# Kernel optimization log

Hardware: AMD Instinct MI355X
Metric: run time of the kernel (lower is better)

## Reference

```python
import jax, jax.numpy as jnp
import numpy as np

N = 50000        # nodes
E = 800000       # edges (avg degree 16)
H = 128          # hidden_nf
IN_NODE = 11     # in_node_nf
IN_EDGE = 4      # in_edge_nf
L = 4            # n_layers


def _lin_init(key, fan_in, fan_out, layers=None):
    shape = (fan_in, fan_out) if layers is None else (layers, fan_in, fan_out)
    return jax.random.normal(key, shape, dtype=jnp.float32) / np.sqrt(fan_in)


def setup_inputs() -> dict:
    key = jax.random.key(0)
    ks = jax.random.split(key, 16)
    edge_in = 2 * H + 1 + IN_EDGE   # [h_row, h_col, radial, edge_attr]
    node_in = H + H + IN_NODE       # [h, agg, h0]
    return {
        "h0": jax.random.normal(ks[0], (N, IN_NODE), dtype=jnp.float32),
        "x": jax.random.normal(ks[1], (N, 3), dtype=jnp.float32),
        "edge_index": jax.random.randint(ks[2], (2, E), 0, N),
        "edge_attr": jax.random.normal(ks[3], (E, IN_EDGE), dtype=jnp.float32),
        "node_mask": jnp.ones((N, 1), dtype=jnp.float32),
        "edge_mask": jnp.ones((E, 1), dtype=jnp.float32),
        "n_nodes": N,
        "emb_w": _lin_init(ks[4], IN_NODE, H),
        "emb_b": jnp.zeros((H,), dtype=jnp.float32),
        "ew1": _lin_init(ks[5], edge_in, H, L),
        "eb1": jnp.zeros((L, H), dtype=jnp.float32),
        "ew2": _lin_init(ks[6], H, H, L),
        "eb2": jnp.zeros((L, H), dtype=jnp.float32),
        "nw1": _lin_init(ks[7], node_in, H, L),
        "nb1": jnp.zeros((L, H), dtype=jnp.float32),
        "nw2": _lin_init(ks[8], H, H, L),
        "nb2": jnp.zeros((L, H), dtype=jnp.float32),
    }


def reference(h0, x, edge_index, edge_attr, node_mask, edge_mask, n_nodes,
              emb_w, emb_b, ew1, eb1, ew2, eb2, nw1, nb1, nw2, nb2):
    row, col = edge_index[0], edge_index[1]
    num_nodes = h0.shape[0]
    # coord2radial (coords never updated since coord_model is not called)
    coord_diff = x[row] - x[col]                               # [E, 3]
    radial = jnp.sum(coord_diff * coord_diff, axis=1, keepdims=True)  # [E, 1]

    h = h0 @ emb_w + emb_b                                     # embedding, [N, H]
    for i in range(L):
        # edge model
        edge_in = jnp.concatenate([h[row], h[col], radial, edge_attr], axis=1)
        m = jax.nn.silu(edge_in @ ew1[i] + eb1[i])
        m = jax.nn.silu(m @ ew2[i] + eb2[i])
        m = m * edge_mask                                      # [E, H]
        # node model: scatter-sum messages, concat with h and node_attr=h0
        agg = jax.ops.segment_sum(m, row, num_segments=num_nodes)  # [N, H]
        node_in = jnp.concatenate([h, agg, h0], axis=1)
        out = jax.nn.silu(node_in @ nw1[i] + nb1[i]) @ nw2[i] + nb2[i]
        h = h + out                                            # recurrent residual
    return h
```

## Files before the change

### kernel.cpp

```cpp
#include <hip/hip_runtime.h>

#define NN 50000
#define NE 800000
#define HD 128
#define INN 11
#define NL 4
#define NG16 3125
#define BTS 132
#define K1S 292

typedef __attribute__((ext_vector_type(8))) short bf16x8;
typedef __attribute__((ext_vector_type(4))) float f32x4;

__device__ __forceinline__ float silu_f(float x) {
    return x * __builtin_amdgcn_rcpf(1.0f + __expf(-x));
}

__device__ __forceinline__ short f2bf(float x) {
    unsigned u = __float_as_uint(x);
    return (short)((u + 0x7FFFu + ((u >> 16) & 1u)) >> 16);
}
__device__ __forceinline__ unsigned f2bf2u(float lo, float hi) {
    unsigned a = __float_as_uint(lo), b = __float_as_uint(hi);
    a = (a + 0x7FFFu + ((a >> 16) & 1u)) >> 16;
    b = (b + 0x7FFFu + ((b >> 16) & 1u)) & 0xFFFF0000u;
    return a | b;
}
__device__ __forceinline__ bf16x8 pack8(float4 a, float4 b) {
    bf16x8 r;
    r[0] = f2bf(a.x); r[1] = f2bf(a.y); r[2] = f2bf(a.z); r[3] = f2bf(a.w);
    r[4] = f2bf(b.x); r[5] = f2bf(b.y); r[6] = f2bf(b.z); r[7] = f2bf(b.w);
    return r;
}

__global__ __launch_bounds__(256) void embed_kernel(
    const float* __restrict__ h0, const float* __restrict__ w,
    const float* __restrict__ b, float* __restrict__ h)
{
    int idx = blockIdx.x * 256 + threadIdx.x;
    if (idx >= NN * HD) return;
    int n = idx >> 7, j = idx & 127;
    float acc = b[j];
    #pragma unroll
    for (int k = 0; k < INN; ++k)
        acc += h0[n * INN + k] * w[k * HD + j];
    h[idx] = acc;
}

__global__ __launch_bounds__(256) void csr_zero(int* __restrict__ cnt)
{
    int i = blockIdx.x * 256 + threadIdx.x;
    if (i < NN) cnt[i] = 0;
}

__global__ __launch_bounds__(256) void csr_hist(const int* __restrict__ ei, int* __restrict__ cnt)
{
    int e = blockIdx.x * 256 + threadIdx.x;
    atomicAdd(&cnt[ei[e]], 1);
}

__global__ __launch_bounds__(1024) void csr_scan(
    const int* __restrict__ cnt, int* __restrict__ rowptr, int* __restrict__ cursor)
{
    __shared__ int part[1024];
    int t = threadIdx.x;
    int base = t * 49;
    int s = 0;
    for (int i = 0; i < 49; ++i) { int j = base + i; if (j < NN) s += cnt[j]; }
    part[t] = s;
    __syncthreads();
    for (int off = 1; off < 1024; off <<= 1) {
        int v = (t >= off) ? part[t - off] : 0;
        __syncthreads();
        part[t] += v;
        __syncthreads();
    }
    int run = (t == 0) ? 0 : part[t - 1];
    for (int i = 0; i < 49; ++i) {
        int j = base + i;
        if (j < NN) { rowptr[j] = run; cursor[j] = run; run += cnt[j]; }
    }
    if (t == 1023) rowptr[NN] = part[1023];
}

__global__ __launch_bounds__(256) void csr_fill(
    const int* __restrict__ ei, int* __restrict__ cursor, int* __restrict__ eidx)
{
    int e = blockIdx.x * 256 + threadIdx.x;
    int r = ei[e];
    int p = atomicAdd(&cursor[r], 1);
    eidx[p] = e;
}

__global__ __launch_bounds__(256) void edge_pre(
    const int* __restrict__ ei, const int* __restrict__ eidx,
    const float* __restrict__ x, const float* __restrict__ eattr,
    const float* __restrict__ emask,
    int4* __restrict__ ed_p, float4* __restrict__ ea_p)
{
    int p = blockIdx.x * 256 + threadIdx.x;
    int e = eidx[p];
    int r = ei[e], c = ei[NE + e];
    float dx = x[3 * r]     - x[3 * c];
    float dy = x[3 * r + 1] - x[3 * c + 1];
    float dz = x[3 * r + 2] - x[3 * c + 2];
    float rad = dx * dx + dy * dy + dz * dz;
    ed_p[p] = make_int4(r * 64, c * 64, __float_as_int(rad), __float_as_int(emask[e]));
    ea_p[p] = ((const float4*)eattr)[e];
}

__global__ __launch_bounds__(512) void tu_mfma(
    const float* __restrict__ h, const float* __restrict__ ew1_l,
    short* __restrict__ tb, short* __restrict__ ub)
{
    __shared__ __align__(16) short BT[128 * BTS];
    const float* wsrc = ew1_l + (blockIdx.y ? 128 * HD : 0);
    short* outp = blockIdx.y ? ub : tb;
    for (int i = threadIdx.x; i < 128 * 128; i += 512) {
        int c = i >> 7, k = i & 127;
        BT[c * BTS + k] = f2bf(wsrc[k * HD + c]);
    }
    int wv = threadIdx.x >> 6, lane = threadIdx.x & 63;
    int ln15 = lane & 15, quad = lane >> 4;
    __syncthreads();

    for (int g = blockIdx.x * 8 + wv; g < NG16; g += gridDim.x * 8) {
        int row = g * 16 + ln15;
        const float* hrow = h + row * HD;
        bf16x8 afr[4];
        #pragma unroll
        for (int kt = 0; kt < 4; ++kt) {
            float4 x0 = *(const float4*)(hrow + kt * 32 + quad * 8);
            float4 x1 = *(const float4*)(hrow + kt * 32 + quad * 8 + 4);
            afr[kt] = pack8(x0, x1);
        }
        #pragma unroll
        for (int ct = 0; ct < 8; ++ct) {
            f32x4 acc = {0.f, 0.f, 0.f, 0.f};
            #pragma unroll
            for (int kt = 0; kt < 4; ++kt) {
                bf16x8 bfr = *(const bf16x8*)&BT[(ct * 16 + ln15) * BTS + kt * 32 + quad * 8];
                acc = __builtin_amdgcn_mfma_f32_16x16x32_bf16(afr[kt], bfr, acc, 0, 0, 0);
            }
            int col = ct * 16 + ln15;
            #pragma unroll
            for (int r4 = 0; r4 < 4; ++r4) {
                int orow = g * 16 + quad * 4 + r4;
                outp[orow * HD + col] = f2bf(acc[r4]);
            }
        }
    }
}

__global__ __launch_bounds__(512) void edge_m_kernel(
    const short* __restrict__ tb, const short* __restrict__ ub,
    const int4* __restrict__ ed_p, const float4* __restrict__ ea_p,
    const int* __restrict__ rowptr,
    const float* __restrict__ ew1_l, const float* __restrict__ eb1_l,
    const float* __restrict__ ew2_l, const float* __restrict__ eb2_l,
    float* __restrict__ agg)
{
    __shared__ __align__(16) short BT[128 * BTS];
    __shared__ __align__(16) short VA[8][16 * BTS];
    __shared__ float s_b2[128];

    for (int i = threadIdx.x; i < 128 * 128; i += 512) {
        int k = i >> 7, n = i & 127;
        BT[n * BTS + k] = f2bf(ew2_l[i]);
    }
    if (threadIdx.x < 128) s_b2[threadIdx.x] = eb2_l[threadIdx.x];

    int cp = threadIdx.x & 63;
    int c0 = cp * 2;
    float wr0  = ew1_l[256 * HD + c0],     wr1  = ew1_l[256 * HD + c0 + 1];
    float wa00 = ew1_l[257 * HD + c0],     wa01 = ew1_l[257 * HD + c0 + 1];
    float wa10 = ew1_l[258 * HD + c0],     wa11 = ew1_l[258 * HD + c0 + 1];
    float wa20 = ew1_l[259 * HD + c0],     wa21 = ew1_l[259 * HD + c0 + 1];
    float wa30 = ew1_l[260 * HD + c0],     wa31 = ew1_l[260 * HD + c0 + 1];
    float b10  = eb1_l[c0],                b11  = eb1_l[c0 + 1];

    int lane = threadIdx.x & 63;
    int wv   = threadIdx.x >> 6;
    int ln15 = lane & 15;
    int quad = lane >> 4;
    short* VAw = &VA[wv][0];
    const unsigned* tb32 = (const unsigned*)tb;
    const unsigned* ub32 = (const unsigned*)ub;
    __syncthreads();

    for (int n = blockIdx.x * 8 + wv; n < NN; n += gridDim.x * 8) {
        int s = rowptr[n], e = rowptr[n + 1];
        unsigned tw = tb32[n * 64 + cp];
        float t0 = __uint_as_float(tw << 16);
        float t1 = __uint_as_float(tw & 0xFFFF0000u);

        float sums[8];
        #pragma unroll
        for (int ct = 0; ct < 8; ++ct) sums[ct] = 0.f;

        for (int base = s; base < e; base += 16) {
            #pragma unroll 4
            for (int i = 0; i < 16; ++i) {
                int p = base + i;
                unsigned out = 0u;
                if (p < e) {
                    int4   ed = ed_p[p];
                    float4 ea = ea_p[p];
                    float rad = __int_as_float(ed.z);
                    unsigned uw = ub32[ed.y + cp];
                    float u0 = __uint_as_float(uw << 16);
                    float u1 = __uint_as_float(uw & 0xFFFF0000u);
                    float base0 = rad * wr0 + ea.x * wa00 + ea.y * wa10 + ea.z * wa20 + ea.w * wa30 + b10;
                    float base1 = rad * wr1 + ea.x * wa01 + ea.y * wa11 + ea.z * wa21 + ea.w * wa31 + b11;
                    out = f2bf2u(silu_f(t0 + u0 + base0), silu_f(t1 + u1 + base1));
                }
                *(unsigned*)&VAw[i * BTS + c0] = out;
            }

            int pr = base + quad * 4;
            float mk0 = (pr + 0 < e) ? __int_as_float(ed_p[pr + 0].w) : 0.f;
            float mk1 = (pr + 1 < e) ? __int_as_float(ed_p[pr + 1].w) : 0.f;
            float mk2 = (pr + 2 < e) ? __int_as_float(ed_p[pr + 2].w) : 0.f;
            float mk3 = (pr + 3 < e) ? __int_as_float(ed_p[pr + 3].w) : 0.f;

            __builtin_amdgcn_wave_barrier();
            __builtin_amdgcn_s_waitcnt(0xc07f);

            bf16x8 afr[4];
            #pragma unroll
            for (int kt = 0; kt < 4; ++kt)
                afr[kt] = *(const bf16x8*)&VAw[ln15 * BTS + kt * 32 + quad * 8];

            __builtin_amdgcn_wave_barrier();

            #pragma unroll
            for (int ct = 0; ct < 8; ++ct) {
                f32x4 acc = {0.f, 0.f, 0.f, 0.f};
                #pragma unroll
                for (int kt = 0; kt < 4; ++kt) {
                    bf16x8 bfr = *(const bf16x8*)&BT[(ct * 16 + ln15) * BTS + kt * 32 + quad * 8];
                    acc = __builtin_amdgcn_mfma_f32_16x16x32_bf16(afr[kt], bfr, acc, 0, 0, 0);
                }
                float b2c = s_b2[ct * 16 + ln15];
                sums[ct] += silu_f(acc[0] + b2c) * mk0 + silu_f(acc[1] + b2c) * mk1
                          + silu_f(acc[2] + b2c) * mk2 + silu_f(acc[3] + b2c) * mk3;
            }
        }

        #pragma unroll
        for (int ct = 0; ct < 8; ++ct) {
            float v = sums[ct];
            v += __shfl_xor(v, 16, 64);
            v += __shfl_xor(v, 32, 64);
            sums[ct] = v;
        }
        float vA = (quad & 2) ? ((quad & 1) ? sums[6] : sums[4])
                              : ((quad & 1) ? sums[2] : sums[0]);
        float vB = (quad & 2) ? ((quad & 1) ? sums[7] : sums[5])
                              : ((quad & 1) ? sums[3] : sums[1]);
        int colA = quad * 32 + ln15;
        agg[n * HD + colA]      = vA;
        agg[n * HD + colA + 16] = vB;
    }
}

__global__ __launch_bounds__(512) void nk1_mfma(
    const float* __restrict__ h, const float* __restrict__ agg,
    const float* __restrict__ h0,
    const float* __restrict__ nw1_l, const float* __restrict__ nb1_l,
    short* __restrict__ qb)
{
    __shared__ __align__(16) short BT[64 * K1S];
    int c0 = blockIdx.y * 64;
    for (int i = threadIdx.x; i < 64 * 288; i += 512) {
        int c = i / 288, k = i - c * 288;
        BT[c * K1S + k] = (k < 267) ? f2bf(nw1_l[k * HD + c0 + c]) : (short)0;
    }
    int wv = threadIdx.x >> 6, lane = threadIdx.x & 63;
    int ln15 = lane & 15, quad = lane >> 4;
    __syncthreads();

    for (int g = blockIdx.x * 8 + wv; g < NG16; g += gridDim.x * 8) {
        int row = g * 16 + ln15;
        const float* hrow = h + row * HD;
        const float* arow = agg + row * HD;
        bf16x8 afr[9];
        #pragma unroll
        for (int kt = 0; kt < 4; ++kt) {
            float4 x0 = *(const float4*)(hrow + kt * 32 + quad * 8);
            float4 x1 = *(const float4*)(hrow + kt * 32 + quad * 8 + 4);
            afr[kt] = pack8(x0, x1);
        }
        #pragma unroll
        for (int kt = 0; kt < 4; ++kt) {
            float4 x0 = *(const float4*)(arow + kt * 32 + quad * 8);
            float4 x1 = *(const float4*)(arow + kt * 32 + quad * 8 + 4);
            afr[4 + kt] = pack8(x0, x1);
        }
        {
            bf16x8 a8 = {0, 0, 0, 0, 0, 0, 0, 0};
            if (quad == 0) {
                #pragma unroll
                for (int jj = 0; jj < 8; ++jj) a8[jj] = f2bf(h0[row * INN + jj]);
            } else if (quad == 1) {
                #pragma unroll
                for (int jj = 0; jj < 3; ++jj) a8[jj] = f2bf(h0[row * INN + 8 + jj]);
            }
            afr[8] = a8;
        }
        #pragma unroll
        for (int ct = 0; ct < 4; ++ct) {
            f32x4 acc = {0.f, 0.f, 0.f, 0.f};
            #pragma unroll
            for (int kt = 0; kt < 9; ++kt) {
                bf16x8 bfr = *(const bf16x8*)&BT[(ct * 16 + ln15) * K1S + kt * 32 + quad * 8];
                acc = __builtin_amdgcn_mfma_f32_16x16x32_bf16(afr[kt], bfr, acc, 0, 0, 0);
            }
            int col = c0 + ct * 16 + ln15;
            float b = nb1_l[col];
            #pragma unroll
            for (int r4 = 0; r4 < 4; ++r4) {
                int orow = g * 16 + quad * 4 + r4;
                qb[orow * HD + col] = f2bf(silu_f(acc[r4] + b));
            }
        }
    }
}

__global__ __launch_bounds__(512) void nk2_mfma(
    const short* __restrict__ qb, const float* __restrict__ nw2_l,
    const float* __restrict__ nb2_l, float* __restrict__ h)
{
    __shared__ __align__(16) short BT[128 * BTS];
    for (int i = threadIdx.x; i < 128 * 128; i += 512) {
        int c = i >> 7, k = i & 127;
        BT[c * BTS + k] = f2bf(nw2_l[k * HD + c]);
    }
    int wv = threadIdx.x >> 6, lane = threadIdx.x & 63;
    int ln15 = lane & 15, quad = lane >> 4;
    __syncthreads();

    for (int g = blockIdx.x * 8 + wv; g < NG16; g += gridDim.x * 8) {
        int row = g * 16 + ln15;
        bf16x8 afr[4];
        #pragma unroll
        for (int kt = 0; kt < 4; ++kt)
            afr[kt] = *(const bf16x8*)(qb + row * HD + kt * 32 + quad * 8);

        #pragma unroll
        for (int ct = 0; ct < 8; ++ct) {
            f32x4 acc = {0.f, 0.f, 0.f, 0.f};
            #pragma unroll
            for (int kt = 0; kt < 4; ++kt) {
                bf16x8 bfr = *(const bf16x8*)&BT[(ct * 16 + ln15) * BTS + kt * 32 + quad * 8];
                acc = __builtin_amdgcn_mfma_f32_16x16x32_bf16(afr[kt], bfr, acc, 0, 0, 0);
            }
            int col = ct * 16 + ln15;
            float b = nb2_l[col];
            #pragma unroll
            for (int r4 = 0; r4 < 4; ++r4) {
                int orow = g * 16 + quad * 4 + r4;
                h[orow * HD + col] += acc[r4] + b;
            }
        }
    }
}

extern "C" void kernel_launch(void* const* d_in, const int* in_sizes, int n_in,
                              void* d_out, int out_size, void* d_ws, size_t ws_size,
                              hipStream_t stream)
{
    const float* h0    = (const float*)d_in[0];
    const float* x     = (const float*)d_in[1];
    const int*   ei    = (const int*)d_in[2];
    const float* eattr = (const float*)d_in[3];
    const float* emask = (const float*)d_in[5];
    const float* emb_w = (const float*)d_in[7];
    const float* emb_b = (const float*)d_in[8];
    const float* ew1   = (const float*)d_in[9];
    const float* eb1   = (const float*)d_in[10];
    const float* ew2   = (const float*)d_in[11];
    const float* eb2   = (const float*)d_in[12];
    const float* nw1   = (const float*)d_in[13];
    const float* nb1   = (const float*)d_in[14];
    const float* nw2   = (const float*)d_in[15];
    const float* nb2   = (const float*)d_in[16];

    float* h = (float*)d_out;

    short*  tb     = (short*)d_ws;
    short*  ub     = tb + (size_t)NN * HD;
    float*  agg    = (float*)(ub + (size_t)NN * HD);
    short*  qb     = tb;
    int*    cnt    = (int*)(agg + (size_t)NN * HD);
    int*    rowptr = cnt + NN;
    int*    cursor = rowptr + NN + 1;
    int*    eidx   = cursor + NN;
    int4*   ed_p   = (int4*)(eidx + NE + 1);
    float4* ea_p   = (float4*)(ed_p + NE);

    csr_zero<<<(NN + 255) / 256, 256, 0, stream>>>(cnt);
    csr_hist<<<NE / 256, 256, 0, stream>>>(ei, cnt);
    csr_scan<<<1, 1024, 0, stream>>>(cnt, rowptr, cursor);
    csr_fill<<<NE / 256, 256, 0, stream>>>(ei, cursor, eidx);
    edge_pre<<<NE / 256, 256, 0, stream>>>(ei, eidx, x, eattr, emask, ed_p, ea_p);

    embed_kernel<<<(NN * HD + 255) / 256, 256, 0, stream>>>(h0, emb_w, emb_b, h);

    dim3 gtu(128, 2);
    dim3 gn1(128, 2);
    for (int l = 0; l < NL; ++l) {
        tu_mfma<<<gtu, 512, 0, stream>>>(h, ew1 + l * 261 * HD, tb, ub);
        edge_m_kernel<<<512, 512, 0, stream>>>(tb, ub, ed_p, ea_p, rowptr,
            ew1 + l * 261 * HD, eb1 + l * HD, ew2 + l * HD * HD, eb2 + l * HD, agg);
        nk1_mfma<<<gn1, 512, 0, stream>>>(h, agg, h0,
            nw1 + l * 267 * HD, nb1 + l * HD, qb);
        nk2_mfma<<<128, 512, 0, stream>>>(qb, nw2 + l * HD * HD, nb2 + l * HD, h);
    }
}
```

Baseline: 1.552 ms.

## Software-prefetch next chunk's gathered neighbor features before MFMA in edge kernel

Moves the edge-index load and the dependent gather of neighbor features (ub) for the next 16 edges ahead of the current chunk's MFMA work, holding them in registers (uwv, radv). The aim is to hide the latency of the dependent global gather behind matrix compute. Mask loads are hoisted to the top of each chunk, and the launch bounds gain a min-blocks hint of 4, which caps registers per thread. Holding 32 extra live values under a tighter register cap risks spills.

```diff
diff --git a/kernel.cpp b/kernel.cpp
--- a/kernel.cpp
+++ b/kernel.cpp
@@ -152,7 +152,7 @@
     }
 }
 
-__global__ __launch_bounds__(512) void edge_m_kernel(
+__global__ __launch_bounds__(512, 4) void edge_m_kernel(
     const short* __restrict__ tb, const short* __restrict__ ub,
     const int4* __restrict__ ed_p, const float4* __restrict__ ea_p,
     const int* __restrict__ rowptr,
@@ -189,7 +189,7 @@
     __syncthreads();
 
     for (int n = blockIdx.x * 8 + wv; n < NN; n += gridDim.x * 8) {
-        int s = rowptr[n], e = rowptr[n + 1];
+        int s = rowptr[n], en = rowptr[n + 1];
         unsigned tw = tb32[n * 64 + cp];
         float t0 = __uint_as_float(tw << 16);
         float t1 = __uint_as_float(tw & 0xFFFF0000u);
@@ -198,31 +198,39 @@
         #pragma unroll
         for (int ct = 0; ct < 8; ++ct) sums[ct] = 0.f;
 
-        for (int base = s; base < e; base += 16) {
-            #pragma unroll 4
+        unsigned uwv[16];
+        float    radv[16];
+
+        #pragma unroll
+        for (int i = 0; i < 16; ++i) {
+            int p = s + i;
+            int4 ed = (p < en) ? ed_p[p] : make_int4(0, 0, 0, 0);
+            radv[i] = __int_as_float(ed.z);
+            uwv[i]  = ub32[ed.y + cp];
+        }
+
+        for (int base = s; base < en; base += 16) {
+            int pr = base + quad * 4;
+            float mk0 = (pr + 0 < en) ? __int_as_float(ed_p[pr + 0].w) : 0.f;
+            float mk1 = (pr + 1 < en) ? __int_as_float(ed_p[pr + 1].w) : 0.f;
+            float mk2 = (pr + 2 < en) ? __int_as_float(ed_p[pr + 2].w) : 0.f;
+            float mk3 = (pr + 3 < en) ? __int_as_float(ed_p[pr + 3].w) : 0.f;
+
+            #pragma unroll
             for (int i = 0; i < 16; ++i) {
                 int p = base + i;
                 unsigned out = 0u;
-                if (p < e) {
-                    int4   ed = ed_p[p];
+                if (p < en) {
                     float4 ea = ea_p[p];
-                    float rad = __int_as_float(ed.z);
-                    unsigned uw = ub32[ed.y + cp];
-                    float u0 = __uint_as_float(uw << 16);
-                    float u1 = __uint_as_float(uw & 0xFFFF0000u);
-                    float base0 = rad * wr0 + ea.x * wa00 + ea.y * wa10 + ea.z * wa20 + ea.w * wa30 + b10;
-                    float base1 = rad * wr1 + ea.x * wa01 + ea.y * wa11 + ea.z * wa21 + ea.w * wa31 + b11;
+                    float u0 = __uint_as_float(uwv[i] << 16);
+                    float u1 = __uint_as_float(uwv[i] & 0xFFFF0000u);
+                    float base0 = radv[i] * wr0 + ea.x * wa00 + ea.y * wa10 + ea.z * wa20 + ea.w * wa30 + b10;
+                    float base1 = radv[i] * wr1 + ea.x * wa01 + ea.y * wa11 + ea.z * wa21 + ea.w * wa31 + b11;
                     out = f2bf2u(silu_f(t0 + u0 + base0), silu_f(t1 + u1 + base1));
                 }
                 *(unsigned*)&VAw[i * BTS + c0] = out;
             }
 
-            int pr = base + quad * 4;
-            float mk0 = (pr + 0 < e) ? __int_as_float(ed_p[pr + 0].w) : 0.f;
-            float mk1 = (pr + 1 < e) ? __int_as_float(ed_p[pr + 1].w) : 0.f;
-            float mk2 = (pr + 2 < e) ? __int_as_float(ed_p[pr + 2].w) : 0.f;
-            float mk3 = (pr + 3 < e) ? __int_as_float(ed_p[pr + 3].w) : 0.f;
-
             __builtin_amdgcn_wave_barrier();
             __builtin_amdgcn_s_waitcnt(0xc07f);
 
@@ -232,6 +240,17 @@
                 afr[kt] = *(const bf16x8*)&VAw[ln15 * BTS + kt * 32 + quad * 8];
 
             __builtin_amdgcn_wave_barrier();
+
+            int nb = base + 16;
+            if (nb < en) {
+                #pragma unroll
+                for (int i = 0; i < 16; ++i) {
+                    int p = nb + i;
+                    int4 ed = (p < en) ? ed_p[p] : make_int4(0, 0, 0, 0);
+                    radv[i] = __int_as_float(ed.z);
+                    uwv[i]  = ub32[ed.y + cp];
+                }
+            }
 
             #pragma unroll
             for (int ct = 0; ct < 8; ++ct) {
```

New measurement: 1.589 ms. +2.3%, slower.
